# Optimization experiments

Hardware: AMD Instinct MI355X
Metric: run time of the kernel (lower is better)

## Reference

```python
import jax, jax.numpy as jnp
import numpy as np

TMP = 1.0  # temperature from init

def setup_inputs() -> dict:
    key = jax.random.key(0)
    k1, k2, k3 = jax.random.split(key, 3)
    B, D, C = 8192, 1024, 4096
    x = jax.random.normal(k1, (B, D), dtype=jnp.float32)
    mod = jax.random.normal(k2, (B, D), dtype=jnp.float32)
    W = jax.random.normal(k3, (C, D), dtype=jnp.float32) * 0.02  # cls.weight
    return {"x": x, "mod": mod, "W": W}

def reference(x, mod, W):
    # att = softmax(mod / tmp, axis=1) + 1, shape (B, D)
    att = jax.nn.softmax(mod / TMP, axis=1) + 1.0
    # result[b, c] = sum_d W[c, d] * att[b, d] * x[b, d]
    # == (att * x) @ W.T  -- collapses the repeat + per-sample matvec loop
    return jnp.einsum('bd,cd->bc', att * x, W)
```

## Files before the change

kernel.cpp:

```cpp
#include <hip/hip_runtime.h>
#include <hip/hip_bf16.h>
#include <cstdint>
#include <cstddef>

typedef __bf16 bf16_t;
typedef __bf16 bf16x8 __attribute__((ext_vector_type(8)));
typedef __bf16 bf16x4 __attribute__((ext_vector_type(4)));
typedef float  f32x4  __attribute__((ext_vector_type(4)));

#define KDIM 1024
#define NT   16
#define NTT  32

__global__ void prep_kernel(const float* __restrict__ x,
                            const float* __restrict__ mod,
                            const float* __restrict__ W,
                            bf16_t* __restrict__ a,
                            bf16_t* __restrict__ Wb,
                            int D, int Bn) {
  if ((int)blockIdx.x >= Bn) {
    const size_t i = (((size_t)blockIdx.x - Bn) * blockDim.x + threadIdx.x) * 8;
    float4 u = *(const float4*)(W + i);
    float4 v = *(const float4*)(W + i + 4);
    bf16x8 o;
    o[0] = (bf16_t)u.x; o[1] = (bf16_t)u.y; o[2] = (bf16_t)u.z; o[3] = (bf16_t)u.w;
    o[4] = (bf16_t)v.x; o[5] = (bf16_t)v.y; o[6] = (bf16_t)v.z; o[7] = (bf16_t)v.w;
    *(bf16x8*)(Wb + i) = o;
    return;
  }

  const int b = blockIdx.x;
  const int t = threadIdx.x;
  const size_t row = (size_t)b * D;

  float4 mv = ((const float4*)(mod + row))[t];
  float mx = fmaxf(fmaxf(mv.x, mv.y), fmaxf(mv.z, mv.w));
#pragma unroll
  for (int o = 32; o > 0; o >>= 1) mx = fmaxf(mx, __shfl_xor(mx, o));

  __shared__ float redmax[4];
  __shared__ float redsum[4];
  const int wave = t >> 6, lane = t & 63;
  if (lane == 0) redmax[wave] = mx;
  __syncthreads();
  mx = fmaxf(fmaxf(redmax[0], redmax[1]), fmaxf(redmax[2], redmax[3]));

  float4 e;
  e.x = __expf(mv.x - mx); e.y = __expf(mv.y - mx);
  e.z = __expf(mv.z - mx); e.w = __expf(mv.w - mx);
  float s = (e.x + e.y) + (e.z + e.w);
#pragma unroll
  for (int o = 32; o > 0; o >>= 1) s += __shfl_xor(s, o);
  if (lane == 0) redsum[wave] = s;
  __syncthreads();
  s = (redsum[0] + redsum[1]) + (redsum[2] + redsum[3]);

  const float inv = 1.0f / s;
  float4 xv = ((const float4*)(x + row))[t];
  bf16x4 o4;
  o4[0] = (bf16_t)((e.x * inv + 1.0f) * xv.x);
  o4[1] = (bf16_t)((e.y * inv + 1.0f) * xv.y);
  o4[2] = (bf16_t)((e.z * inv + 1.0f) * xv.z);
  o4[3] = (bf16_t)((e.w * inv + 1.0f) * xv.w);
  *((bf16x4*)(a + row) + t) = o4;
}

__global__ __launch_bounds__(512, 2) void gemm256_kernel(
    const bf16_t* __restrict__ A, const bf16_t* __restrict__ B,
    float* __restrict__ C, int M, int N) {
  __shared__ __align__(16) bf16_t lds[2 * 32768];

  const int tid  = threadIdx.x;
  const int wave = tid >> 6;
  const int lane = tid & 63;
  const int quad = lane >> 4;
  const int l16  = lane & 15;
  const int wm   = wave >> 2;
  const int wn   = wave & 3;

  const int nwg = gridDim.x;
  int flat = blockIdx.x;
  flat = (flat & 7) * (nwg >> 3) + (flat >> 3);
  const int mpairs = M >> 9;
  const int m0 = (flat % mpairs) << 9;
  const int n0 = (flat / mpairs) << 8;

  const int trow = tid >> 3;
  const int colg = (tid & 7) ^ (trow & 7);
  const bf16_t* aSrc = A + (size_t)(m0 + trow) * KDIM + colg * 8;
  const bf16_t* bSrc = B + (size_t)(n0 + trow) * KDIM + colg * 8;
  const int ldsW = wave * 512;

#define GLDS(src_, dst_) __builtin_amdgcn_global_load_lds( \
      (const __attribute__((address_space(1))) void*)(src_), \
      (__attribute__((address_space(3))) void*)(dst_), 16, 0, 0)

#define ISSUE_A(h, t_) do { \
      const bf16_t* s_ = aSrc + (size_t)((((t_) >> 4) * 256) + (h) * 128) * KDIM + ((t_) & 15) * 64; \
      bf16_t* d_ = lds + ((t_) & 1) * 32768 + (h) * 8192 + ldsW; \
      GLDS(s_, d_); \
      GLDS(s_ + (size_t)64 * KDIM, d_ + 4096); \
    } while (0)

#define ISSUE_B(h, t_) do { \
      const bf16_t* s_ = bSrc + (size_t)((h) * 128) * KDIM + ((t_) & 15) * 64; \
      bf16_t* d_ = lds + ((t_) & 1) * 32768 + 16384 + (h) * 8192 + ldsW; \
      GLDS(s_, d_); \
      GLDS(s_ + (size_t)64 * KDIM, d_ + 4096); \
    } while (0)

  ISSUE_A(0, 0); ISSUE_A(1, 0);
  ISSUE_B(0, 0); ISSUE_B(1, 0);
  ISSUE_B(0, 1); ISSUE_B(1, 1);

  f32x4 acc[8][4];
#pragma unroll
  for (int i = 0; i < 8; ++i)
#pragma unroll
    for (int j = 0; j < 4; ++j) acc[i][j] = (f32x4){0.f, 0.f, 0.f, 0.f};

  const int aBase = (wm * 128 + l16) * 64;
  const int bBase = (wn * 64 + l16) * 64;
  const int c0 = ((quad)     ^ (l16 & 7)) * 8;
  const int c1 = ((4 + quad) ^ (l16 & 7)) * 8;

  asm volatile("s_waitcnt vmcnt(4)" ::: "memory");
  __builtin_amdgcn_s_barrier();

  bf16x8 bfr[4][2];

#define PHASE(q_, ISSUE_STMT, WAIT_STMT) do { \
      bf16x8 af[2][2]; \
      _Pragma("unroll") \
      for (int i = 0; i < 2; ++i) { \
        af[i][0] = *(const bf16x8*)(At + aBase + ((q_) * 32 + i * 16) * 64 + c0); \
        af[i][1] = *(const bf16x8*)(At + aBase + ((q_) * 32 + i * 16) * 64 + c1); \
      } \
      ISSUE_STMT; \
      asm volatile("" ::: "memory"); \
      __builtin_amdgcn_s_barrier(); \
      asm volatile("s_waitcnt lgkmcnt(0)" ::: "memory"); \
      __builtin_amdgcn_s_setprio(1); \
      _Pragma("unroll") \
      for (int i = 0; i < 2; ++i) \
        _Pragma("unroll") \
        for (int j = 0; j < 4; ++j) { \
          acc[(q_) * 2 + i][j] = __builtin_amdgcn_mfma_f32_16x16x32_bf16( \
              af[i][0], bfr[j][0], acc[(q_) * 2 + i][j], 0, 0, 0); \
          acc[(q_) * 2 + i][j] = __builtin_amdgcn_mfma_f32_16x16x32_bf16( \
              af[i][1], bfr[j][1], acc[(q_) * 2 + i][j], 0, 0, 0); \
        } \
      __builtin_amdgcn_s_setprio(0); \
      WAIT_STMT; \
      asm volatile("" ::: "memory"); \
      __builtin_amdgcn_s_barrier(); \
    } while (0)

#define FLUSH(mrep_) do { \
      _Pragma("unroll") \
      for (int ri = 0; ri < 8; ++ri) { \
        const int mg = m0 + (mrep_) * 256 + wm * 128 + ri * 16 + quad * 4; \
        _Pragma("unroll") \
        for (int j = 0; j < 4; ++j) { \
          const int ng = n0 + wn * 64 + j * 16 + l16; \
          _Pragma("unroll") \
          for (int r = 0; r < 4; ++r) \
            C[(size_t)(mg + r) * N + ng] = acc[ri][j][r]; \
        } \
      } \
    } while (0)

#pragma unroll 1
  for (int t = 0; t < NTT; ++t) {
    const bf16_t* At = lds + (t & 1) * 32768;
    const bf16_t* Bt = At + 16384;

#pragma unroll
    for (int j = 0; j < 4; ++j) {
      bfr[j][0] = *(const bf16x8*)(Bt + bBase + j * 16 * 64 + c0);
      bfr[j][1] = *(const bf16x8*)(Bt + bBase + j * 16 * 64 + c1);
    }
    PHASE(0, if (t + 1 < NTT) ISSUE_A(0, t + 1), (void)0);
    PHASE(1, if (t + 1 < NTT) ISSUE_A(1, t + 1), (void)0);
    PHASE(2, if (t + 2 < NTT) ISSUE_B(0, t + 2), (void)0);
    PHASE(3, if (t + 2 < NTT) ISSUE_B(1, t + 2),
          if (t < NTT - 2) { asm volatile("s_waitcnt vmcnt(4)" ::: "memory"); }
          else             { asm volatile("s_waitcnt vmcnt(0)" ::: "memory"); });

    if (t == NT - 1) {
      FLUSH(0);
#pragma unroll
      for (int i = 0; i < 8; ++i)
#pragma unroll
        for (int j = 0; j < 4; ++j) acc[i][j] = (f32x4){0.f, 0.f, 0.f, 0.f};
    }
  }

  FLUSH(1);
}

extern "C" void kernel_launch(void* const* d_in, const int* in_sizes, int n_in,
                              void* d_out, int out_size, void* d_ws, size_t ws_size,
                              hipStream_t stream) {
  const float* x   = (const float*)d_in[0];
  const float* mod = (const float*)d_in[1];
  const float* W   = (const float*)d_in[2];
  float* out = (float*)d_out;

  const int D = 1024;
  const int Bn = in_sizes[0] / D;
  const int Cn = in_sizes[2] / D;

  bf16_t* a  = (bf16_t*)d_ws;
  bf16_t* Wb = (bf16_t*)((char*)d_ws + (size_t)Bn * D * sizeof(bf16_t));

  const int castBlocks = (Cn * D) / (256 * 8);
  prep_kernel<<<Bn + castBlocks, 256, 0, stream>>>(x, mod, W, a, Wb, D, Bn);

  const int nwg = (Bn / 512) * (Cn / 256);
  gemm256_kernel<<<nwg, 512, 0, stream>>>(a, Wb, out, Bn, Cn);
}
```

Measured before the change: 272.9 us.

## Interleave first-half C tile stores with next tiles' MFMA phases

Instead of flushing all 128 accumulator registers for the first M half in one block after tile 15, the stores are split into pairs of rows and placed inside the phases of tiles 15 and 16, with vmcnt waits raised to account for the outstanding stores. This is meant to overlap the global store traffic with MFMA compute and avoid a stall at the mid-kernel boundary. It relies on careful vmcnt counting: a wrong count could read stale LDS data, and the extra stores in flight may slow the loads they share the queue with.

```diff
diff --git a/kernel.cpp b/kernel.cpp
--- a/kernel.cpp
+++ b/kernel.cpp
@@ -129,7 +129,31 @@
 
   bf16x8 bfr[4][2];
 
-#define PHASE(q_, ISSUE_STMT, WAIT_STMT) do { \
+#define BPANEL(Bt_) do { \
+      _Pragma("unroll") \
+      for (int j = 0; j < 4; ++j) { \
+        bfr[j][0] = *(const bf16x8*)((Bt_) + bBase + j * 16 * 64 + c0); \
+        bfr[j][1] = *(const bf16x8*)((Bt_) + bBase + j * 16 * 64 + c1); \
+      } \
+    } while (0)
+
+#define FLUSH_PAIR(r0_) do { \
+      _Pragma("unroll") \
+      for (int ri = (r0_); ri < (r0_) + 2; ++ri) { \
+        const int mg = m0 + wm * 128 + ri * 16 + quad * 4; \
+        _Pragma("unroll") \
+        for (int j = 0; j < 4; ++j) { \
+          const int ng = n0 + wn * 64 + j * 16 + l16; \
+          _Pragma("unroll") \
+          for (int r = 0; r < 4; ++r) \
+            C[(size_t)(mg + r) * N + ng] = acc[ri][j][r]; \
+        } \
+        _Pragma("unroll") \
+        for (int j = 0; j < 4; ++j) acc[ri][j] = (f32x4){0.f, 0.f, 0.f, 0.f}; \
+      } \
+    } while (0)
+
+#define PHASE(q_, ISSUE_STMT, PREWAIT_STMT, WAIT_STMT, POSTWAIT_STMT) do { \
       bf16x8 af[2][2]; \
       _Pragma("unroll") \
       for (int i = 0; i < 2; ++i) { \
@@ -151,52 +175,65 @@
               af[i][1], bfr[j][1], acc[(q_) * 2 + i][j], 0, 0, 0); \
         } \
       __builtin_amdgcn_s_setprio(0); \
+      PREWAIT_STMT; \
       WAIT_STMT; \
+      POSTWAIT_STMT; \
       asm volatile("" ::: "memory"); \
       __builtin_amdgcn_s_barrier(); \
     } while (0)
 
-#define FLUSH(mrep_) do { \
-      _Pragma("unroll") \
-      for (int ri = 0; ri < 8; ++ri) { \
-        const int mg = m0 + (mrep_) * 256 + wm * 128 + ri * 16 + quad * 4; \
-        _Pragma("unroll") \
-        for (int j = 0; j < 4; ++j) { \
-          const int ng = n0 + wn * 64 + j * 16 + l16; \
-          _Pragma("unroll") \
-          for (int r = 0; r < 4; ++r) \
-            C[(size_t)(mg + r) * N + ng] = acc[ri][j][r]; \
-        } \
-      } \
+#define TILE_STD(t_) do { \
+      const bf16_t* At = lds + ((t_) & 1) * 32768; \
+      const bf16_t* Bt = At + 16384; \
+      BPANEL(Bt); \
+      PHASE(0, if ((t_) + 1 < NTT) ISSUE_A(0, (t_) + 1), (void)0, (void)0, (void)0); \
+      PHASE(1, if ((t_) + 1 < NTT) ISSUE_A(1, (t_) + 1), (void)0, (void)0, (void)0); \
+      PHASE(2, if ((t_) + 2 < NTT) ISSUE_B(0, (t_) + 2), (void)0, (void)0, (void)0); \
+      PHASE(3, if ((t_) + 2 < NTT) ISSUE_B(1, (t_) + 2), (void)0, \
+            if ((t_) < NTT - 2) { asm volatile("s_waitcnt vmcnt(4)" ::: "memory"); } \
+            else                { asm volatile("s_waitcnt vmcnt(0)" ::: "memory"); }, \
+            (void)0); \
     } while (0)
 
 #pragma unroll 1
-  for (int t = 0; t < NTT; ++t) {
-    const bf16_t* At = lds + (t & 1) * 32768;
+  for (int t = 0; t < 15; ++t) TILE_STD(t);
+
+  {
+    const bf16_t* At = lds + 32768;
     const bf16_t* Bt = At + 16384;
-
+    BPANEL(Bt);
+    PHASE(0, ISSUE_A(0, 16), (void)0, (void)0, (void)0);
+    PHASE(1, ISSUE_A(1, 16), (void)0, (void)0, (void)0);
+    PHASE(2, ISSUE_B(0, 17), FLUSH_PAIR(0), (void)0, (void)0);
+    PHASE(3, ISSUE_B(1, 17), (void)0,
+          asm volatile("s_waitcnt vmcnt(36)" ::: "memory"),
+          FLUSH_PAIR(2));
+  }
+  {
+    const bf16_t* At = lds;
+    const bf16_t* Bt = At + 16384;
+    BPANEL(Bt);
+    PHASE(0, ISSUE_A(0, 17), FLUSH_PAIR(4), (void)0, (void)0);
+    PHASE(1, ISSUE_A(1, 17), FLUSH_PAIR(6), (void)0, (void)0);
+    PHASE(2, ISSUE_B(0, 18), (void)0, (void)0, (void)0);
+    PHASE(3, ISSUE_B(1, 18), (void)0,
+          asm volatile("s_waitcnt vmcnt(36)" ::: "memory"), (void)0);
+  }
+
+#pragma unroll 1
+  for (int t = 17; t < NTT; ++t) TILE_STD(t);
+
+#pragma unroll
+  for (int ri = 0; ri < 8; ++ri) {
+    const int mg = m0 + 256 + wm * 128 + ri * 16 + quad * 4;
 #pragma unroll
     for (int j = 0; j < 4; ++j) {
-      bfr[j][0] = *(const bf16x8*)(Bt + bBase + j * 16 * 64 + c0);
-      bfr[j][1] = *(const bf16x8*)(Bt + bBase + j * 16 * 64 + c1);
+      const int ng = n0 + wn * 64 + j * 16 + l16;
+#pragma unroll
+      for (int r = 0; r < 4; ++r)
+        C[(size_t)(mg + r) * N + ng] = acc[ri][j][r];
     }
-    PHASE(0, if (t + 1 < NTT) ISSUE_A(0, t + 1), (void)0);
-    PHASE(1, if (t + 1 < NTT) ISSUE_A(1, t + 1), (void)0);
-    PHASE(2, if (t + 2 < NTT) ISSUE_B(0, t + 2), (void)0);
-    PHASE(3, if (t + 2 < NTT) ISSUE_B(1, t + 2),
-          if (t < NTT - 2) { asm volatile("s_waitcnt vmcnt(4)" ::: "memory"); }
-          else             { asm volatile("s_waitcnt vmcnt(0)" ::: "memory"); });
-
-    if (t == NT - 1) {
-      FLUSH(0);
-#pragma unroll
-      for (int i = 0; i < 8; ++i)
-#pragma unroll
-        for (int j = 0; j < 4; ++j) acc[i][j] = (f32x4){0.f, 0.f, 0.f, 0.f};
-    }
-  }
-
-  FLUSH(1);
+  }
 }
 
 extern "C" void kernel_launch(void* const* d_in, const int* in_sizes, int n_in,
```

New measurement: 256.7 us. 1.06x faster.

## Drop paired M-tiles per workgroup and double-buffer A fragment register reads

Applied to the files above, without the earlier changes.

Each workgroup now computes a single 256x256 output tile instead of two M-tiles that shared a B panel, which doubles the grid and drops the mid-loop flush and accumulator reset. The tile mapping changes from M-major to N-major ordering. Each phase now prefetches the next A fragments from LDS into a second register set while the current MFMAs run, using partial lgkmcnt waits and a sched_barrier. This overlaps LDS reads with MFMA work but gives up the B-panel reuse of the paired tiles and may raise register pressure.

```diff
diff --git a/kernel.cpp b/kernel.cpp
--- a/kernel.cpp
+++ b/kernel.cpp
@@ -10,7 +10,6 @@
 
 #define KDIM 1024
 #define NT   16
-#define NTT  32
 
 __global__ void prep_kernel(const float* __restrict__ x,
                             const float* __restrict__ mod,
@@ -81,9 +80,9 @@
   const int nwg = gridDim.x;
   int flat = blockIdx.x;
   flat = (flat & 7) * (nwg >> 3) + (flat >> 3);
-  const int mpairs = M >> 9;
-  const int m0 = (flat % mpairs) << 9;
-  const int n0 = (flat / mpairs) << 8;
+  const int ntiles = N >> 8;
+  const int m0 = (flat / ntiles) << 8;
+  const int n0 = (flat % ntiles) << 8;
 
   const int trow = tid >> 3;
   const int colg = (tid & 7) ^ (trow & 7);
@@ -96,14 +95,14 @@
       (__attribute__((address_space(3))) void*)(dst_), 16, 0, 0)
 
 #define ISSUE_A(h, t_) do { \
-      const bf16_t* s_ = aSrc + (size_t)((((t_) >> 4) * 256) + (h) * 128) * KDIM + ((t_) & 15) * 64; \
+      const bf16_t* s_ = aSrc + (size_t)((h) * 128) * KDIM + (t_) * 64; \
       bf16_t* d_ = lds + ((t_) & 1) * 32768 + (h) * 8192 + ldsW; \
       GLDS(s_, d_); \
       GLDS(s_ + (size_t)64 * KDIM, d_ + 4096); \
     } while (0)
 
 #define ISSUE_B(h, t_) do { \
-      const bf16_t* s_ = bSrc + (size_t)((h) * 128) * KDIM + ((t_) & 15) * 64; \
+      const bf16_t* s_ = bSrc + (size_t)((h) * 128) * KDIM + (t_) * 64; \
       bf16_t* d_ = lds + ((t_) & 1) * 32768 + 16384 + (h) * 8192 + ldsW; \
       GLDS(s_, d_); \
       GLDS(s_ + (size_t)64 * KDIM, d_ + 4096); \
@@ -128,75 +127,82 @@
   __builtin_amdgcn_s_barrier();
 
   bf16x8 bfr[4][2];
-
-#define PHASE(q_, ISSUE_STMT, WAIT_STMT) do { \
-      bf16x8 af[2][2]; \
+  bf16x8 afA[2][2], afB[2][2];
+
+#define BPANEL(Bt_) do { \
+      _Pragma("unroll") \
+      for (int j = 0; j < 4; ++j) { \
+        bfr[j][0] = *(const bf16x8*)((Bt_) + bBase + j * 16 * 64 + c0); \
+        bfr[j][1] = *(const bf16x8*)((Bt_) + bBase + j * 16 * 64 + c1); \
+      } \
+    } while (0)
+
+#define RD_AF(S_, q_) do { \
       _Pragma("unroll") \
       for (int i = 0; i < 2; ++i) { \
-        af[i][0] = *(const bf16x8*)(At + aBase + ((q_) * 32 + i * 16) * 64 + c0); \
-        af[i][1] = *(const bf16x8*)(At + aBase + ((q_) * 32 + i * 16) * 64 + c1); \
+        S_[i][0] = *(const bf16x8*)(At + aBase + ((q_) * 32 + i * 16) * 64 + c0); \
+        S_[i][1] = *(const bf16x8*)(At + aBase + ((q_) * 32 + i * 16) * 64 + c1); \
       } \
-      ISSUE_STMT; \
-      asm volatile("" ::: "memory"); \
-      __builtin_amdgcn_s_barrier(); \
-      asm volatile("s_waitcnt lgkmcnt(0)" ::: "memory"); \
-      __builtin_amdgcn_s_setprio(1); \
+    } while (0)
+
+#define MFMA16(q_, S_) do { \
       _Pragma("unroll") \
       for (int i = 0; i < 2; ++i) \
         _Pragma("unroll") \
         for (int j = 0; j < 4; ++j) { \
           acc[(q_) * 2 + i][j] = __builtin_amdgcn_mfma_f32_16x16x32_bf16( \
-              af[i][0], bfr[j][0], acc[(q_) * 2 + i][j], 0, 0, 0); \
+              S_[i][0], bfr[j][0], acc[(q_) * 2 + i][j], 0, 0, 0); \
           acc[(q_) * 2 + i][j] = __builtin_amdgcn_mfma_f32_16x16x32_bf16( \
-              af[i][1], bfr[j][1], acc[(q_) * 2 + i][j], 0, 0, 0); \
+              S_[i][1], bfr[j][1], acc[(q_) * 2 + i][j], 0, 0, 0); \
         } \
-      __builtin_amdgcn_s_setprio(0); \
-      WAIT_STMT; \
+    } while (0)
+
+#define PH(qcur_, SCUR_, SNXT_, qnxt_, ISSUE_STMT, LGKM_STR, END_STMT) do { \
+      if ((qnxt_) >= 0) { RD_AF(SNXT_, ((qnxt_) & 3)); } \
+      ISSUE_STMT; \
       asm volatile("" ::: "memory"); \
       __builtin_amdgcn_s_barrier(); \
-    } while (0)
-
-#define FLUSH(mrep_) do { \
-      _Pragma("unroll") \
-      for (int ri = 0; ri < 8; ++ri) { \
-        const int mg = m0 + (mrep_) * 256 + wm * 128 + ri * 16 + quad * 4; \
-        _Pragma("unroll") \
-        for (int j = 0; j < 4; ++j) { \
-          const int ng = n0 + wn * 64 + j * 16 + l16; \
-          _Pragma("unroll") \
-          for (int r = 0; r < 4; ++r) \
-            C[(size_t)(mg + r) * N + ng] = acc[ri][j][r]; \
-        } \
-      } \
+      asm volatile(LGKM_STR ::: "memory"); \
+      __builtin_amdgcn_sched_barrier(0); \
+      __builtin_amdgcn_s_setprio(1); \
+      MFMA16(qcur_, SCUR_); \
+      __builtin_amdgcn_s_setprio(0); \
+      END_STMT; \
+      asm volatile("" ::: "memory"); \
+      __builtin_amdgcn_s_barrier(); \
     } while (0)
 
 #pragma unroll 1
-  for (int t = 0; t < NTT; ++t) {
+  for (int t = 0; t < NT; ++t) {
     const bf16_t* At = lds + (t & 1) * 32768;
     const bf16_t* Bt = At + 16384;
 
+    BPANEL(Bt);
+    RD_AF(afA, 0);
+
+    PH(0, afA, afB, 1, if (t + 1 < NT) ISSUE_A(0, t + 1),
+       "s_waitcnt lgkmcnt(4)", (void)0);
+    PH(1, afB, afA, 2, if (t + 1 < NT) ISSUE_A(1, t + 1),
+       "s_waitcnt lgkmcnt(4)", (void)0);
+    PH(2, afA, afB, 3, if (t + 2 < NT) ISSUE_B(0, t + 2),
+       "s_waitcnt lgkmcnt(4)", (void)0);
+    PH(3, afB, afA, -1, if (t + 2 < NT) ISSUE_B(1, t + 2),
+       "s_waitcnt lgkmcnt(0)",
+       if (t < NT - 2) { asm volatile("s_waitcnt vmcnt(4)" ::: "memory"); }
+       else            { asm volatile("s_waitcnt vmcnt(0)" ::: "memory"); });
+  }
+
+#pragma unroll
+  for (int ri = 0; ri < 8; ++ri) {
+    const int mg = m0 + wm * 128 + ri * 16 + quad * 4;
 #pragma unroll
     for (int j = 0; j < 4; ++j) {
-      bfr[j][0] = *(const bf16x8*)(Bt + bBase + j * 16 * 64 + c0);
-      bfr[j][1] = *(const bf16x8*)(Bt + bBase + j * 16 * 64 + c1);
-    }
-    PHASE(0, if (t + 1 < NTT) ISSUE_A(0, t + 1), (void)0);
-    PHASE(1, if (t + 1 < NTT) ISSUE_A(1, t + 1), (void)0);
-    PHASE(2, if (t + 2 < NTT) ISSUE_B(0, t + 2), (void)0);
-    PHASE(3, if (t + 2 < NTT) ISSUE_B(1, t + 2),
-          if (t < NTT - 2) { asm volatile("s_waitcnt vmcnt(4)" ::: "memory"); }
-          else             { asm volatile("s_waitcnt vmcnt(0)" ::: "memory"); });
-
-    if (t == NT - 1) {
-      FLUSH(0);
-#pragma unroll
-      for (int i = 0; i < 8; ++i)
-#pragma unroll
-        for (int j = 0; j < 4; ++j) acc[i][j] = (f32x4){0.f, 0.f, 0.f, 0.f};
+      const int ng = n0 + wn * 64 + j * 16 + l16;
+#pragma unroll
+      for (int r = 0; r < 4; ++r)
+        C[(size_t)(mg + r) * N + ng] = acc[ri][j][r];
     }
   }
-
-  FLUSH(1);
 }
 
 extern "C" void kernel_launch(void* const* d_in, const int* in_sizes, int n_in,
@@ -217,6 +223,6 @@
   const int castBlocks = (Cn * D) / (256 * 8);
   prep_kernel<<<Bn + castBlocks, 256, 0, stream>>>(x, mod, W, a, Wb, D, Bn);
 
-  const int nwg = (Bn / 512) * (Cn / 256);
+  const int nwg = (Bn / 256) * (Cn / 256);
   gemm256_kernel<<<nwg, 512, 0, stream>>>(a, Wb, out, Bn, Cn);
 }
```

After: 256.2 us. -6.1%, faster.
